# Kernel optimization log

Hardware: AMD Instinct MI355X
Metric: run time of the kernel (lower is better)

Reference implementation:

```python
import jax, jax.numpy as jnp
import numpy as np

P = 64        # patch size
NATOMS = 256  # dictionary atoms
N = 262144    # signal length
K = 262081    # npatches = N - P + 1 (stride-1 sliding patches)
M = 512       # measurement rows of A


def setup_inputs() -> dict:
    key = jax.random.key(0)
    k0, k1, k2, k3, k4, k5, k6 = jax.random.split(key, 7)
    d = jax.random.normal(k0, (1, P, NATOMS), jnp.float32) * 0.1
    x = jax.random.normal(k1, (NATOMS, K), jnp.float32) * 0.1
    ss = jnp.zeros((N, 1), jnp.float32)  # only its shape is used
    vb = (jax.random.uniform(k2, (N, 1)) > 0.05).astype(jnp.float32)
    # stride-1 sliding-window patch indices: column k covers [k, k+P)
    patches = (jnp.arange(K, dtype=jnp.int32)[None, :]
               + jnp.arange(P, dtype=jnp.int32)[:, None])  # [P, K]
    # npp = number of patches covering each signal sample
    npp = jnp.zeros((N, 1), jnp.float32).at[patches.reshape(-1), 0].add(1.0)
    sRef = jax.random.normal(k3, (N, 1), jnp.float32)
    A = jax.random.normal(k4, (M, N), jnp.float32) * 0.01
    Tarr = jax.random.normal(k5, (M, 1), jnp.float32)
    meanY = jnp.float32(0.1)
    ds = jax.random.normal(k6, (N, 1), jnp.float32)
    lam2 = jnp.float32(0.5)
    return {"d": d, "x": x, "ss": ss, "vb": vb, "patches": patches,
            "npp": npp, "sRef": sRef, "A": A, "Tarr": Tarr,
            "meanY": meanY, "ds": ds, "lam2": lam2, "npatches": K}


def reference(d, x, ss, vb, patches, npp, sRef, A, Tarr, meanY, ds, lam2, npatches):
    # ss_b[p, k] = (D @ X)[p, k] + meanY  -> per-patch reconstructions
    ss_b = jnp.squeeze(d) @ x + meanY                      # [P, K]
    # vectorized scatter-add replacing the torch loop over npatches
    ss_p_sum = jnp.zeros_like(ss).at[patches.reshape(-1), 0].add(ss_b.reshape(-1))  # [N,1]
    ss_f = (lam2 * ds + ss_p_sum) / (lam2 + npp)           # [N,1]
    ss_masked = ss_f * vb                                  # [N,1]
    Tref = A @ (ss_masked + sRef)                          # [M,1]
    return jnp.mean((Tref - Tarr) ** 2)
```

## Files before the change

### kernel.cpp

```cpp
#include <hip/hip_runtime.h>


namespace {
constexpr int kP = 64;
constexpr int kA = 256;
constexpr int kN = 262144;
constexpr int kK = 262081;
constexpr int kM = 512;

constexpr int CB = 256;
constexpr int OPT = 16;
constexpr int NB = CB * OPT;
constexpr int NCHUNK = kN / NB;
constexpr int NSPLIT = 16;
constexpr int APS = kA / NSPLIT;
constexpr int XS_LOG = NB + 64;
constexpr int XS_L4 = XS_LOG / 4;
constexpr int XS_P4 = 1304;
constexpr int R4 = XS_L4 + 1;
constexpr int GV_CH = 8;

static_assert(APS == 16, "transpose loop assumes APS==16");

__device__ __forceinline__ float f4c(const float4& v, int i) {
  switch (i & 3) {
    case 0: return v.x;
    case 1: return v.y;
    case 2: return v.z;
    default: return v.w;
  }
}

__device__ __forceinline__ void stage_row(const float* __restrict__ x,
                                          float* __restrict__ xsf,
                                          int a, int n0, int rlo, int rhi) {
  const int SA = (a + 1) & 3;
  const int gf = a * kK + n0 - 63 - SA;
  const int g4base = gf >> 2;
  const float4* __restrict__ x4 = (const float4*)x;
  const int g4max = (kA * kK) / 4 - 1;
  float4 vals[5];
#pragma unroll
  for (int u = 0; u < 5; ++u) {
    int r = (int)threadIdx.x + u * CB;
    if (r < R4) {
      int g4 = g4base + r;
      g4 = g4 < 0 ? 0 : (g4 > g4max ? g4max : g4);
      vals[u] = x4[g4];
    }
  }
#pragma unroll
  for (int u = 0; u < 5; ++u) {
    int r = (int)threadIdx.x + u * CB;
    if (r >= R4) continue;
    if (r >= rlo && r < rhi) {
      const int i0 = 4 * r - SA;
#pragma unroll
      for (int w = 0; w < 4; ++w) {
        int i = i0 + w;
        xsf[i + 4 * (i >> 4)] = f4c(vals[u], w);
      }
    } else {
#pragma unroll
      for (int w = 0; w < 4; ++w) {
        int i = 4 * r + w - SA;
        if ((unsigned)i < (unsigned)XS_LOG) {
          int k = n0 - 63 + i;
          float f = ((unsigned)k < (unsigned)kK) ? f4c(vals[u], w) : 0.0f;
          xsf[i + 4 * (i >> 4)] = f;
        }
      }
    }
  }
}

__device__ __forceinline__ void compute_atom(const float4* __restrict__ xs4,
                                             const float4* __restrict__ dt4,
                                             int a_loc, float* __restrict__ acc) {
  const int t4 = threadIdx.x * 4;
  float4 w[5];
#pragma unroll
  for (int q = 0; q < 4; ++q) {
    int l4 = t4 + q;
    w[q] = xs4[l4 + (l4 >> 2)];
  }
#pragma unroll
  for (int c = 0; c < 16; ++c) {
    {
      int l4 = t4 + c + 4;
      w[(c + 4) % 5] = xs4[l4 + (l4 >> 2)];
    }
    float4 D = dt4[a_loc * 16 + 15 - c];
    float dc[4] = {D.w, D.z, D.y, D.x};
#pragma unroll
    for (int i = 0; i < 4; ++i) {
      float coef = dc[i];
#pragma unroll
      for (int j = 0; j < OPT; ++j) {
        int off = i + j;
        float xv = f4c(w[(c + (off >> 2)) % 5], off & 3);
        acc[j] = fmaf(coef, xv, acc[j]);
      }
    }
  }
}

__global__ __launch_bounds__(CB, 3) void conv_kernel(const float* __restrict__ d,
                                                     const float* __restrict__ x,
                                                     float* __restrict__ part) {
  __shared__ float4 xsA[XS_P4];
  __shared__ float4 xsB[XS_P4];
  __shared__ float4 dt4[APS * 16];
  const int n0 = blockIdx.x * NB;
  const int a0 = blockIdx.y * APS;
  const int tid = threadIdx.x;
  const int rlo = (blockIdx.x == 0) ? 17 : 1;
  const int rhi = (blockIdx.x == NCHUNK - 1) ? 1024 : 1040;

  float* dtf = (float*)dt4;
#pragma unroll 1
  for (int i = tid; i < APS * kP; i += CB) {
    int al = i & (APS - 1);
    int p = i >> 4;
    dtf[al * kP + p] = d[p * kA + a0 + al];
  }

  float acc[OPT];
#pragma unroll
  for (int j = 0; j < OPT; ++j) acc[j] = 0.0f;

  stage_row(x, (float*)xsA, a0, n0, rlo, rhi);
  __syncthreads();

#pragma unroll 1
  for (int a = 0; a < APS; a += 2) {
    stage_row(x, (float*)xsB, a0 + a + 1, n0, rlo, rhi);
    compute_atom(xsA, dt4, a, acc);
    __syncthreads();
    if (a + 2 < APS) stage_row(x, (float*)xsA, a0 + a + 2, n0, rlo, rhi);
    compute_atom(xsB, dt4, a + 1, acc);
    __syncthreads();
  }

  float4* outp = (float4*)(part + (size_t)blockIdx.y * kN + n0 + tid * OPT);
#pragma unroll
  for (int j = 0; j < 4; ++j)
    outp[j] = make_float4(acc[4 * j], acc[4 * j + 1], acc[4 * j + 2], acc[4 * j + 3]);
}

__global__ void vmask_kernel(const float* __restrict__ part, const float* __restrict__ ds,
                             const float* __restrict__ npp, const float* __restrict__ vb,
                             const float* __restrict__ sRef,
                             const float* __restrict__ pMeanY,
                             const float* __restrict__ pLam2, float* __restrict__ v) {
  const int i = blockIdx.x * blockDim.x + threadIdx.x;
  const float meanY = pMeanY[0];
  const float lam2 = pLam2[0];
  float4 s = make_float4(0.f, 0.f, 0.f, 0.f);
#pragma unroll
  for (int c = 0; c < NSPLIT; ++c) {
    float4 p = ((const float4*)(part + (size_t)c * kN))[i];
    s.x += p.x; s.y += p.y; s.z += p.z; s.w += p.w;
  }
  const float4 dd = ((const float4*)ds)[i];
  const float4 np = ((const float4*)npp)[i];
  const float4 vbv = ((const float4*)vb)[i];
  const float4 sr = ((const float4*)sRef)[i];
  float4 r;
  r.x = (lam2 * dd.x + s.x + meanY * np.x) / (lam2 + np.x) * vbv.x + sr.x;
  r.y = (lam2 * dd.y + s.y + meanY * np.y) / (lam2 + np.y) * vbv.y + sr.y;
  r.z = (lam2 * dd.z + s.z + meanY * np.z) / (lam2 + np.z) * vbv.z + sr.z;
  r.w = (lam2 * dd.w + s.w + meanY * np.w) / (lam2 + np.w) * vbv.w + sr.w;
  ((float4*)v)[i] = r;
}

__global__ __launch_bounds__(256) void gemv_kernel(const float* __restrict__ A,
                                                   const float* __restrict__ v,
                                                   float* __restrict__ Tp) {
  const int m = blockIdx.x >> 3;
  const int ch = blockIdx.x & (GV_CH - 1);
  const float4* __restrict__ A4 = (const float4*)(A + (size_t)m * kN);
  const float4* __restrict__ v4 = (const float4*)v;
  const int b0 = ch * (kN / 4 / GV_CH) + threadIdx.x;
  float s = 0.0f;
#pragma unroll 8
  for (int r = 0; r < 32; ++r) {
    float4 av = A4[b0 + r * 256];
    float4 vv = v4[b0 + r * 256];
    s = fmaf(av.x, vv.x, s);
    s = fmaf(av.y, vv.y, s);
    s = fmaf(av.z, vv.z, s);
    s = fmaf(av.w, vv.w, s);
  }
#pragma unroll
  for (int o = 32; o > 0; o >>= 1) s += __shfl_down(s, o, 64);
  __shared__ float red[4];
  if ((threadIdx.x & 63) == 0) red[threadIdx.x >> 6] = s;
  __syncthreads();
  if (threadIdx.x == 0) Tp[blockIdx.x] = red[0] + red[1] + red[2] + red[3];
}

__global__ void loss_kernel(const float* __restrict__ Tp, const float* __restrict__ Tarr,
                            float* __restrict__ out) {
  const int tid = threadIdx.x;
  float s = 0.0f;
  for (int m = tid; m < kM; m += 256) {
    float t = 0.0f;
#pragma unroll
    for (int c = 0; c < GV_CH; ++c) t += Tp[m * GV_CH + c];
    float df = t - Tarr[m];
    s = fmaf(df, df, s);
  }
#pragma unroll
  for (int o = 32; o > 0; o >>= 1) s += __shfl_down(s, o, 64);
  __shared__ float red[4];
  if ((tid & 63) == 0) red[tid >> 6] = s;
  __syncthreads();
  if (tid == 0) out[0] = (red[0] + red[1] + red[2] + red[3]) * (1.0f / kM);
}

}

extern "C" void kernel_launch(void* const* d_in, const int* in_sizes, int n_in,
                              void* d_out, int out_size, void* d_ws, size_t ws_size,
                              hipStream_t stream) {
  const float* d    = (const float*)d_in[0];
  const float* x    = (const float*)d_in[1];
  const float* vb   = (const float*)d_in[3];
  const float* npp  = (const float*)d_in[5];
  const float* sRef = (const float*)d_in[6];
  const float* A    = (const float*)d_in[7];
  const float* Tarr = (const float*)d_in[8];
  const float* pMeanY = (const float*)d_in[9];
  const float* ds   = (const float*)d_in[10];
  const float* pLam2 = (const float*)d_in[11];
  float* out = (float*)d_out;

  float* part = (float*)d_ws;
  float* v    = part + (size_t)NSPLIT * kN;
  float* Tp   = v + kN;

  conv_kernel<<<dim3(NCHUNK, NSPLIT), CB, 0, stream>>>(d, x, part);
  vmask_kernel<<<kN / 4 / 256, 256, 0, stream>>>(part, ds, npp, vb, sRef, pMeanY, pLam2, v);
  gemv_kernel<<<kM * GV_CH, 256, 0, stream>>>(A, v, Tp);
  loss_kernel<<<1, 256, 0, stream>>>(Tp, Tarr, out);
}
```

Baseline: 1.130 ms.

## Stage x rows via direct global-to-LDS loads with XOR swizzle and padded filters

Replaces the register-staged row copy with global_load_lds 16-byte transfers straight into shared memory, using an XOR-swizzled layout instead of padding. Filter taps are pre-shifted and zero-padded per atom so the compute loop needs no alignment fixups. Boundary zeroing is done only on the first and last chunks, and occupancy is raised to 4 blocks per CU. This is meant to cut VGPR pressure and staging instruction overhead. In exchange the inner loop does one extra step (17 instead of 16) and edge blocks pay an extra barrier per atom.

```diff
diff --git a/kernel.cpp b/kernel.cpp
--- a/kernel.cpp
+++ b/kernel.cpp
@@ -14,13 +14,11 @@
 constexpr int NCHUNK = kN / NB;
 constexpr int NSPLIT = 16;
 constexpr int APS = kA / NSPLIT;
-constexpr int XS_LOG = NB + 64;
-constexpr int XS_L4 = XS_LOG / 4;
-constexpr int XS_P4 = 1304;
-constexpr int R4 = XS_L4 + 1;
+constexpr int XS4 = 1088;
+constexpr int DPF = 80;
 constexpr int GV_CH = 8;
 
-static_assert(APS == 16, "transpose loop assumes APS==16");
+__device__ __forceinline__ int swz(int l4) { return l4 ^ ((l4 >> 3) & 7); }
 
 __device__ __forceinline__ float f4c(const float4& v, int i) {
   switch (i & 3) {
@@ -31,114 +29,110 @@
   }
 }
 
-__device__ __forceinline__ void stage_row(const float* __restrict__ x,
-                                          float* __restrict__ xsf,
-                                          int a, int n0, int rlo, int rhi) {
+__device__ __forceinline__ void gload_lds16(const void* g, void* l) {
+  __builtin_amdgcn_global_load_lds(
+      (const __attribute__((address_space(1))) unsigned int*)g,
+      (__attribute__((address_space(3))) unsigned int*)l, 16, 0, 0);
+}
+
+__device__ __forceinline__ void stage(const float* __restrict__ x, float4* buf,
+                                      int a, int n0, int tid) {
   const int SA = (a + 1) & 3;
-  const int gf = a * kK + n0 - 63 - SA;
-  const int g4base = gf >> 2;
+  const int g4base = (a * kK + n0 - 63 - SA) >> 2;
+  const int g4max = (kA / 4) * kK - 1;
   const float4* __restrict__ x4 = (const float4*)x;
-  const int g4max = (kA * kK) / 4 - 1;
-  float4 vals[5];
-#pragma unroll
-  for (int u = 0; u < 5; ++u) {
-    int r = (int)threadIdx.x + u * CB;
-    if (r < R4) {
-      int g4 = g4base + r;
-      g4 = g4 < 0 ? 0 : (g4 > g4max ? g4max : g4);
-      vals[u] = x4[g4];
-    }
-  }
-#pragma unroll
-  for (int u = 0; u < 5; ++u) {
-    int r = (int)threadIdx.x + u * CB;
-    if (r >= R4) continue;
-    if (r >= rlo && r < rhi) {
-      const int i0 = 4 * r - SA;
-#pragma unroll
-      for (int w = 0; w < 4; ++w) {
-        int i = i0 + w;
-        xsf[i + 4 * (i >> 4)] = f4c(vals[u], w);
-      }
-    } else {
-#pragma unroll
-      for (int w = 0; w < 4; ++w) {
-        int i = 4 * r + w - SA;
-        if ((unsigned)i < (unsigned)XS_LOG) {
-          int k = n0 - 63 + i;
-          float f = ((unsigned)k < (unsigned)kK) ? f4c(vals[u], w) : 0.0f;
-          xsf[i + 4 * (i >> 4)] = f;
-        }
+  const int wav = tid >> 6, lane = tid & 63;
+  const int sl = lane ^ ((lane >> 3) & 7);
+#pragma unroll
+  for (int r = 0; r < 4; ++r) {
+    const int s = r * 4 + wav;
+    int g4 = g4base + s * 64 + sl;
+    g4 = g4 < 0 ? 0 : (g4 > g4max ? g4max : g4);
+    gload_lds16(x4 + g4, buf + s * 64);
+  }
+  if (tid < 20) {
+    int g4 = g4base + 1024 + (tid ^ ((tid >> 3) & 7));
+    g4 = g4 < 0 ? 0 : (g4 > g4max ? g4max : g4);
+    gload_lds16(x4 + g4, buf + 1024);
+  }
+}
+
+__device__ __forceinline__ void compute_atom(const float4* __restrict__ xs4,
+                                             const float* __restrict__ dpf,
+                                             int al, float* __restrict__ acc) {
+  const int t4 = (int)threadIdx.x * 4;
+  const float4* __restrict__ dp4 = (const float4*)(dpf + al * DPF);
+  float4 w[5];
+#pragma unroll
+  for (int q = 0; q < 4; ++q) w[q] = xs4[swz(t4 + q)];
+#pragma unroll
+  for (int c = 0; c < 17; ++c) {
+    w[(c + 4) % 5] = xs4[swz(t4 + c + 4)];
+    float4 D = dp4[c];
+#pragma unroll
+    for (int i = 0; i < 4; ++i) {
+      float coef = f4c(D, i);
+#pragma unroll
+      for (int j = 0; j < OPT; ++j) {
+        int off = i + j;
+        acc[j] = fmaf(coef, f4c(w[(c + (off >> 2)) % 5], off & 3), acc[j]);
       }
     }
   }
 }
 
-__device__ __forceinline__ void compute_atom(const float4* __restrict__ xs4,
-                                             const float4* __restrict__ dt4,
-                                             int a_loc, float* __restrict__ acc) {
-  const int t4 = threadIdx.x * 4;
-  float4 w[5];
-#pragma unroll
-  for (int q = 0; q < 4; ++q) {
-    int l4 = t4 + q;
-    w[q] = xs4[l4 + (l4 >> 2)];
-  }
-#pragma unroll
-  for (int c = 0; c < 16; ++c) {
-    {
-      int l4 = t4 + c + 4;
-      w[(c + 4) % 5] = xs4[l4 + (l4 >> 2)];
-    }
-    float4 D = dt4[a_loc * 16 + 15 - c];
-    float dc[4] = {D.w, D.z, D.y, D.x};
-#pragma unroll
-    for (int i = 0; i < 4; ++i) {
-      float coef = dc[i];
-#pragma unroll
-      for (int j = 0; j < OPT; ++j) {
-        int off = i + j;
-        float xv = f4c(w[(c + (off >> 2)) % 5], off & 3);
-        acc[j] = fmaf(coef, xv, acc[j]);
-      }
-    }
-  }
-}
-
-__global__ __launch_bounds__(CB, 3) void conv_kernel(const float* __restrict__ d,
+__global__ __launch_bounds__(CB, 4) void conv_kernel(const float* __restrict__ d,
                                                      const float* __restrict__ x,
                                                      float* __restrict__ part) {
-  __shared__ float4 xsA[XS_P4];
-  __shared__ float4 xsB[XS_P4];
-  __shared__ float4 dt4[APS * 16];
+  __shared__ float4 xsA[XS4];
+  __shared__ float4 xsB[XS4];
+  __shared__ float dpf[APS * DPF];
   const int n0 = blockIdx.x * NB;
   const int a0 = blockIdx.y * APS;
   const int tid = threadIdx.x;
-  const int rlo = (blockIdx.x == 0) ? 17 : 1;
-  const int rhi = (blockIdx.x == NCHUNK - 1) ? 1024 : 1040;
-
-  float* dtf = (float*)dt4;
+
+  for (int idx = tid; idx < APS * DPF; idx += CB) {
+    int al = idx / DPF, q = idx - al * DPF;
+    int a = a0 + al, SA = (a + 1) & 3;
+    float v = 0.0f;
+    if (q >= SA && q < SA + 64) v = d[(63 + SA - q) * kA + a];
+    dpf[idx] = v;
+  }
+
+  stage(x, xsA, a0, n0, tid);
+  __syncthreads();
+
+  float acc[OPT];
+#pragma unroll
+  for (int j = 0; j < OPT; ++j) acc[j] = 0.0f;
+
+  const bool first = (blockIdx.x == 0);
+  const bool last = (blockIdx.x == NCHUNK - 1);
+
 #pragma unroll 1
-  for (int i = tid; i < APS * kP; i += CB) {
-    int al = i & (APS - 1);
-    int p = i >> 4;
-    dtf[al * kP + p] = d[p * kA + a0 + al];
-  }
-
-  float acc[OPT];
-#pragma unroll
-  for (int j = 0; j < OPT; ++j) acc[j] = 0.0f;
-
-  stage_row(x, (float*)xsA, a0, n0, rlo, rhi);
-  __syncthreads();
-
-#pragma unroll 1
-  for (int a = 0; a < APS; a += 2) {
-    stage_row(x, (float*)xsB, a0 + a + 1, n0, rlo, rhi);
-    compute_atom(xsA, dt4, a, acc);
-    __syncthreads();
-    if (a + 2 < APS) stage_row(x, (float*)xsA, a0 + a + 2, n0, rlo, rhi);
-    compute_atom(xsB, dt4, a + 1, acc);
+  for (int al = 0; al < APS; ++al) {
+    float4* cur = (al & 1) ? xsB : xsA;
+    float4* nxt = (al & 1) ? xsA : xsB;
+    const int a = a0 + al;
+    if (first | last) {
+      const int SA = (a + 1) & 3;
+      float* curf = (float*)cur;
+      if (first) {
+        if (tid < 63 + SA) {
+          int slot = swz(tid >> 2);
+          curf[slot * 4 + (tid & 3)] = 0.0f;
+        }
+      } else {
+        const int iK = kK - n0 + 63 + SA;
+        for (int i = iK + tid; i < 4176; i += CB) {
+          int slot = swz(i >> 2);
+          curf[slot * 4 + (i & 3)] = 0.0f;
+        }
+      }
+      __syncthreads();
+    }
+    if (al + 1 < APS) stage(x, nxt, a0 + al + 1, n0, tid);
+    compute_atom(cur, dpf, al, acc);
     __syncthreads();
   }
 
```

Result: faster. 913.8 us (-19.2%).
